# Kernel tuning notes

Hardware: AMD Instinct MI355X
Metric: run time of the kernel (lower is better)

Reference implementation:

```python
import jax, jax.numpy as jnp
import numpy as np

METRIC = (1.0, 1.0, 1.0, 1.0, -1.0)  # Cl(4,1) signature
N_HEADS = 8
EPS = 1e-6


def _cayley():
    # Cayley table C[a, b, k]: e_a * e_b = sum_k C[a,b,k] e_k, blades indexed by bitmask over 5 generators.
    C = np.zeros((32, 32, 32), dtype=np.float32)
    for a in range(32):
        for b in range(32):
            s = 0
            t = a >> 1
            while t:
                s += bin(t & b).count('1')
                t >>= 1
            sign = -1.0 if (s & 1) else 1.0
            for i in range(5):
                if (a & b) >> i & 1:
                    sign *= METRIC[i]
            C[a, b, a ^ b] = sign
    return C

_C_NP = _cayley()
GP_MAP = jnp.asarray(_C_NP)  # (32,32,32)
SIG = jnp.asarray(_C_NP[np.arange(32), np.arange(32), 0])  # blade square signs, (32,)


def normalize_cl41(x):
    # normalize each multivector (last-dim 32 blades) to unit RMS
    return x / jnp.sqrt(jnp.mean(x * x, axis=-1, keepdims=True) + EPS)


def versor_linear(x, W):
    # x: (B,S,I,32), W: (O,I,32); out_k = sum_{i,j,l} W[o,i,j] C[j,l,k] x[b,s,i,l]
    O, I, _ = W.shape
    W_op = jnp.einsum('oij,jlk->oilk', W, GP_MAP)  # (O,I,32,32)
    W_mat = W_op.transpose(1, 2, 0, 3).reshape(I * 32, O * 32)
    B, S = x.shape[0], x.shape[1]
    out = (x.reshape(B, S, I * 32) @ W_mat).reshape(B, S, O, 32)
    return normalize_cl41(out)


def versor_attention(x, Wq, Wk, Wv, Wo, lam):
    B, S, D, _ = x.shape
    H = N_HEADS
    hd = D // H

    def split_heads(t):  # (B,S,D,32) -> (B,H,S,hd,32)
        return t.reshape(B, S, H, hd, 32).transpose(0, 2, 1, 3, 4)

    q = split_heads(versor_linear(x, Wq))
    k = split_heads(versor_linear(x, Wk))
    v = split_heads(versor_linear(x, Wv))

    q_flat = (q * SIG).reshape(B, H, S, hd * 32)  # signature-weighted
    k_flat = k.reshape(B, H, S, hd * 32)

    scalar = jnp.einsum('bhsd,bhtd->bhst', q_flat, k_flat)
    scale = 1.0 / jnp.sqrt(jnp.asarray(hd, x.dtype))
    score = scalar * scale

    # torque term: sqrt(relu(|q|^2 |k|^2 - (q.k)^2) + eps) / sqrt(hd)
    q_norm_sq = jnp.sum(q_flat * q_flat, axis=-1)[..., :, None]  # (B,H,S,1)
    k_norm_sq = jnp.sum(k_flat * k_flat, axis=-1)[..., None, :]  # (B,H,1,S)
    torque = jnp.sqrt(jax.nn.relu(q_norm_sq * k_norm_sq - scalar * scalar) + EPS) * scale
    score = score + lam * torque

    probs = jax.nn.softmax(score, axis=-1)
    out = jnp.einsum('bhst,bhtdl->bhsdl', probs, v)  # (B,H,S,hd,32)
    out = out.transpose(0, 2, 1, 3, 4).reshape(B, S, D, 32)
    return versor_linear(out, Wo)


def setup_inputs() -> dict:
    key = jax.random.key(0)
    ks = jax.random.split(key, 5)
    B, S, D = 2, 1024, 128
    std = (2.0 / (D * 32)) ** 0.5  # Versor init
    x = jax.random.normal(ks[0], (B, S, D, 32), jnp.float32)
    Wq = jax.random.normal(ks[1], (D, D, 32), jnp.float32) * std
    Wk = jax.random.normal(ks[2], (D, D, 32), jnp.float32) * std
    Wv = jax.random.normal(ks[3], (D, D, 32), jnp.float32) * std
    Wo = jax.random.normal(ks[4], (D, D, 32), jnp.float32) * std
    attn_lambda = jnp.float32(0.1)
    return {'x': x, 'Wq': Wq, 'Wk': Wk, 'Wv': Wv, 'Wo': Wo, 'attn_lambda': attn_lambda}


def reference(x, Wq, Wk, Wv, Wo, attn_lambda):
    return versor_attention(x, Wq, Wk, Wv, Wo, attn_lambda)
```

## Files before the change

### kernel.cpp

```cpp
#include <hip/hip_runtime.h>
#include <stdint.h>

typedef __attribute__((ext_vector_type(4))) float    f32x4;
typedef __attribute__((ext_vector_type(8))) short    s16x8;
typedef __attribute__((ext_vector_type(4))) short    s16x4;
typedef __attribute__((ext_vector_type(8))) _Float16 f16x8;

#define DEV __device__ __forceinline__

DEV float blade_sign(int a, int b){
    int s = 0, t = a >> 1;
    while (t){ s += __popc(t & b); t >>= 1; }
    float sg = (s & 1) ? -1.0f : 1.0f;
    return ((a & b) & 16) ? -sg : sg;
}
DEV short f2h(float v){
    _Float16 h = (_Float16)v;
    return __builtin_bit_cast(short, h);
}
DEV float h2f(short b){
    return (float)__builtin_bit_cast(_Float16, b);
}

__global__ __launch_bounds__(256) void cast_f32_f16(const float* __restrict__ in,
                                                    short* __restrict__ out){
    const size_t idx = (size_t)blockIdx.x * 256 + threadIdx.x;
    const float4* p = reinterpret_cast<const float4*>(in) + idx * 2;
    float4 a = p[0], b = p[1];
    s16x8 o;
    o[0]=f2h(a.x); o[1]=f2h(a.y); o[2]=f2h(a.z); o[3]=f2h(a.w);
    o[4]=f2h(b.x); o[5]=f2h(b.y); o[6]=f2h(b.z); o[7]=f2h(b.w);
    *reinterpret_cast<s16x8*>(out + idx * 8) = o;
}

__global__ __launch_bounds__(256) void build_wmat(const float* __restrict__ W,
                                                  short* __restrict__ WmT){
    const int idx = blockIdx.x * 256 + threadIdx.x;
    const int n  = idx >> 9;
    const int kg = idx & 511;
    const int o = n >> 5, kb = n & 31;
    const int i = kg >> 2, l0 = (kg & 3) * 8;
    const float* wrow = W + (size_t)(o * 128 + i) * 32;
    s16x8 v;
    #pragma unroll
    for (int e = 0; e < 8; ++e){
        const int l = l0 + e, j = kb ^ l;
        v[e] = f2h(wrow[j] * blade_sign(j, l));
    }
    *reinterpret_cast<s16x8*>(WmT + (size_t)n * 4096 + kg * 8) = v;
}

__global__ __launch_bounds__(256) void row_norms(const short* __restrict__ Q,
                                                 const short* __restrict__ Kq,
                                                 float* __restrict__ Nq,
                                                 float* __restrict__ Nk){
    const int row  = blockIdx.x * 4 + (threadIdx.x >> 6);
    const int lane = threadIdx.x & 63;
    const int b = row >> 13, h = (row >> 10) & 7, s = row & 1023;
    const size_t off = ((size_t)(b * 1024 + s)) * 4096 + h * 512 + lane * 8;
    s16x8 a = *reinterpret_cast<const s16x8*>(Q + off);
    s16x8 c = *reinterpret_cast<const s16x8*>(Kq + off);
    float sq = 0.f, sk = 0.f;
    #pragma unroll
    for (int e = 0; e < 8; ++e){
        float fa = h2f(a[e]); sq = fmaf(fa, fa, sq);
        float fc = h2f(c[e]); sk = fmaf(fc, fc, sk);
    }
    #pragma unroll
    for (int m = 1; m < 64; m <<= 1){
        sq += __shfl_xor(sq, m);
        sk += __shfl_xor(sk, m);
    }
    if (lane == 0){ Nq[row] = sq; Nk[row] = sk; }
}

__global__ __launch_bounds__(256) void softmax_rows(float* __restrict__ Sc){
    const int row  = blockIdx.x * 4 + (threadIdx.x >> 6);
    const int lane = threadIdx.x & 63;
    float* p = Sc + (size_t)row * 1024;
    float v[16];
    float mx = -3.0e38f;
    #pragma unroll
    for (int j = 0; j < 16; ++j){ v[j] = p[lane + j * 64]; mx = fmaxf(mx, v[j]); }
    #pragma unroll
    for (int m = 1; m < 64; m <<= 1) mx = fmaxf(mx, __shfl_xor(mx, m));
    float sum = 0.f;
    #pragma unroll
    for (int j = 0; j < 16; ++j){ v[j] = __expf(v[j] - mx); sum += v[j]; }
    #pragma unroll
    for (int m = 1; m < 64; m <<= 1) sum += __shfl_xor(sum, m);
    const float inv = 1.0f / sum;
    short* pb = reinterpret_cast<short*>(p);
    #pragma unroll
    for (int j = 0; j < 16; ++j) pb[lane + j * 64] = f2h(v[j] * inv);
}

#define GLOAD_LDS(gp, lp) \
    __builtin_amdgcn_global_load_lds( \
        (const __attribute__((address_space(1))) void*)(const void*)(gp), \
        (__attribute__((address_space(3))) void*)(void*)(lp), 16, 0, 0)

template<int EPI>
__global__ __launch_bounds__(256) void versor_gemm(
    const short* __restrict__ Abase, int lda,
    const short* __restrict__ Bbase, int ldb,
    int K, void* __restrict__ OutP,
    const float* __restrict__ NqP, const float* __restrict__ NkP,
    const float* __restrict__ LamP)
{
    __shared__ short As[128 * 32];
    __shared__ short Bs[128 * 32];

    const int tid  = threadIdx.x;
    const int lane = tid & 63;
    const int wid  = tid >> 6;
    const int wr   = wid >> 1;
    const int wc   = wid & 1;
    const int bn = blockIdx.x, bm = blockIdx.y, z = blockIdx.z;

    const short* A = Abase;
    const short* B = Bbase;
    if constexpr (EPI == 4){
        const int b = z >> 3, h = z & 7;
        const size_t off = (size_t)b * 1024 * 4096 + (size_t)h * 512;
        A += off; B += off;
    }
    if constexpr (EPI == 5){
        A += (size_t)z * 1024 * 2048;
        B += (size_t)z * 512 * 1024;
    }

    const int row0 = bm * 128;
    const int col0 = bn * 128;

    const int slot0 = (wid * 2 + 0) * 64 + lane;
    const int slot1 = (wid * 2 + 1) * 64 + lane;
    const int ar0 = slot0 >> 2, ac0 = (slot0 & 3) * 8;
    const int ar1 = slot1 >> 2, ac1 = (slot1 & 3) * 8;
    const short* gA0 = A + (size_t)(row0 + ar0) * lda + ac0;
    const short* gA1 = A + (size_t)(row0 + ar1) * lda + ac1;
    const short* gB0 = B + (size_t)(col0 + ar0) * ldb + ac0;
    const short* gB1 = B + (size_t)(col0 + ar1) * ldb + ac1;
    short* lA0 = As + (wid * 2 + 0) * 512;
    short* lA1 = As + (wid * 2 + 1) * 512;
    short* lB0 = Bs + (wid * 2 + 0) * 512;
    short* lB1 = Bs + (wid * 2 + 1) * 512;

    f32x4 acc[4][4];
    #pragma unroll
    for (int i = 0; i < 4; ++i)
        #pragma unroll
        for (int j = 0; j < 4; ++j)
            acc[i][j] = (f32x4){0.f, 0.f, 0.f, 0.f};

    const int fragoff = (lane & 15) * 32 + (lane >> 4) * 8;

    for (int kt = 0; kt < K; kt += 32){
        __syncthreads();
        GLOAD_LDS(gA0 + kt, lA0);
        GLOAD_LDS(gA1 + kt, lA1);
        GLOAD_LDS(gB0 + kt, lB0);
        GLOAD_LDS(gB1 + kt, lB1);
        __syncthreads();

        f16x8 af[4], bfv[4];
        #pragma unroll
        for (int i = 0; i < 4; ++i){
            af[i]  = *reinterpret_cast<const f16x8*>(As + (wr * 64 + i * 16) * 32 + fragoff);
            bfv[i] = *reinterpret_cast<const f16x8*>(Bs + (wc * 64 + i * 16) * 32 + fragoff);
        }
        #pragma unroll
        for (int mi = 0; mi < 4; ++mi)
            #pragma unroll
            for (int ni = 0; ni < 4; ++ni)
                acc[mi][ni] = __builtin_amdgcn_mfma_f32_16x16x32_f16(
                    af[mi], bfv[ni], acc[mi][ni], 0, 0, 0);
    }

    const int rb = row0 + wr * 64 + (lane >> 4) * 4;
    const int cb = col0 + wc * 64 + (lane & 15);

    if constexpr (EPI <= 3){
        #pragma unroll
        for (int mi = 0; mi < 4; ++mi){
            #pragma unroll
            for (int g = 0; g < 2; ++g){
                f32x4 a0 = acc[mi][2 * g], a1 = acc[mi][2 * g + 1];
                f32x4 ss = a0 * a0 + a1 * a1;
                #pragma unroll
                for (int m = 1; m < 16; m <<= 1){
                    ss.x += __shfl_xor(ss.x, m);
                    ss.y += __shfl_xor(ss.y, m);
                    ss.z += __shfl_xor(ss.z, m);
                    ss.w += __shfl_xor(ss.w, m);
                }
                f32x4 inv;
                inv.x = 1.0f / sqrtf(ss.x * 0.03125f + 1e-6f);
                inv.y = 1.0f / sqrtf(ss.y * 0.03125f + 1e-6f);
                inv.z = 1.0f / sqrtf(ss.z * 0.03125f + 1e-6f);
                inv.w = 1.0f / sqrtf(ss.w * 0.03125f + 1e-6f);
                acc[mi][2 * g]     = a0 * inv;
                acc[mi][2 * g + 1] = a1 * inv;
            }
        }
    }
    if constexpr (EPI == 1){
        const float sg0 = blade_sign(lane & 15, lane & 15);
        const float sg1 = blade_sign(16 | (lane & 15), 16 | (lane & 15));
        #pragma unroll
        for (int mi = 0; mi < 4; ++mi)
            #pragma unroll
            for (int ni = 0; ni < 4; ++ni)
                acc[mi][ni] *= (ni & 1) ? sg1 : sg0;
    }

    if constexpr (EPI == 0 || EPI == 1){
        short* Ob = (short*)OutP;
        #pragma unroll
        for (int mi = 0; mi < 4; ++mi)
            #pragma unroll
            for (int ni = 0; ni < 4; ++ni)
                #pragma unroll
                for (int j = 0; j < 4; ++j)
                    Ob[(size_t)(rb + mi * 16 + j) * 4096 + (cb + ni * 16)] = f2h(acc[mi][ni][j]);
    }
    if constexpr (EPI == 2){
        short* Ob = (short*)OutP;
        #pragma unroll
        for (int mi = 0; mi < 4; ++mi){
            const int r = rb + mi * 16;
            const int b = r >> 10, t = r & 1023;
            #pragma unroll
            for (int ni = 0; ni < 4; ++ni){
                const int c = cb + ni * 16;
                const int h = c >> 9, f = c & 511;
                s16x4 pv;
                #pragma unroll
                for (int j = 0; j < 4; ++j) pv[j] = f2h(acc[mi][ni][j]);
                *reinterpret_cast<s16x4*>(Ob + ((size_t)((b * 8 + h) * 512 + f)) * 1024 + t) = pv;
            }
        }
    }
    if constexpr (EPI == 3){
        float* Of = (float*)OutP;
        #pragma unroll
        for (int mi = 0; mi < 4; ++mi)
            #pragma unroll
            for (int ni = 0; ni < 4; ++ni)
                #pragma unroll
                for (int j = 0; j < 4; ++j)
                    Of[(size_t)(rb + mi * 16 + j) * 4096 + (cb + ni * 16)] = acc[mi][ni][j];
    }
    if constexpr (EPI == 4){
        float* Of = (float*)OutP + (size_t)z * 1024 * 1024;
        const float lam = *LamP;
        const float* nq = NqP + z * 1024;
        const float* nk = NkP + z * 1024;
        #pragma unroll
        for (int mi = 0; mi < 4; ++mi)
            #pragma unroll
            for (int j = 0; j < 4; ++j){
                const int r = rb + mi * 16 + j;
                const float qn = nq[r];
                #pragma unroll
                for (int ni = 0; ni < 4; ++ni){
                    const int c = cb + ni * 16;
                    const float sc = acc[mi][ni][j];
                    const float tq = sqrtf(fmaxf(qn * nk[c] - sc * sc, 0.0f) + 1e-6f);
                    Of[(size_t)r * 1024 + c] = 0.25f * (sc + lam * tq);
                }
            }
    }
    if constexpr (EPI == 5){
        short* Ob = (short*)OutP;
        const int b = z >> 3, h = z & 7;
        #pragma unroll
        for (int mi = 0; mi < 4; ++mi)
            #pragma unroll
            for (int ni = 0; ni < 4; ++ni)
                #pragma unroll
                for (int j = 0; j < 4; ++j)
                    Ob[(size_t)(b * 1024 + rb + mi * 16 + j) * 4096 + h * 512 + (cb + ni * 16)]
                        = f2h(acc[mi][ni][j]);
    }
}

extern "C" void kernel_launch(void* const* d_in, const int* in_sizes, int n_in,
                              void* d_out, int out_size, void* d_ws, size_t ws_size,
                              hipStream_t stream)
{
    (void)in_sizes; (void)n_in; (void)out_size; (void)ws_size;
    const float* x   = (const float*)d_in[0];
    const float* Wq  = (const float*)d_in[1];
    const float* Wk  = (const float*)d_in[2];
    const float* Wv  = (const float*)d_in[3];
    const float* Wo  = (const float*)d_in[4];
    const float* lam = (const float*)d_in[5];
    float* out = (float*)d_out;
    char*  ws  = (char*)d_ws;

    short* Xf  = (short*)(ws);
    short* WmT = (short*)(ws + (16u << 20));
    short* Qf  = (short*)(ws + (48u << 20));
    short* Kf  = (short*)(ws + (64u << 20));
    short* Vt  = (short*)(ws + (80u << 20));
    float* Nq  = (float*)(ws + (96u << 20));
    float* Nk  = (float*)(ws + (96u << 20) + (1u << 20));
    float* Sc  = (float*)(ws + (98u << 20));

    dim3 blk(256);
    cast_f32_f16<<<4096, blk, 0, stream>>>(x, Xf);

    dim3 gproj(32, 16, 1);
    build_wmat<<<8192, blk, 0, stream>>>(Wq, WmT);
    versor_gemm<1><<<gproj, blk, 0, stream>>>(Xf, 4096, WmT, 4096, 4096, Qf, nullptr, nullptr, nullptr);
    build_wmat<<<8192, blk, 0, stream>>>(Wk, WmT);
    versor_gemm<0><<<gproj, blk, 0, stream>>>(Xf, 4096, WmT, 4096, 4096, Kf, nullptr, nullptr, nullptr);
    build_wmat<<<8192, blk, 0, stream>>>(Wv, WmT);
    versor_gemm<2><<<gproj, blk, 0, stream>>>(Xf, 4096, WmT, 4096, 4096, Vt, nullptr, nullptr, nullptr);

    row_norms<<<4096, blk, 0, stream>>>(Qf, Kf, Nq, Nk);

    dim3 gsc(8, 8, 16);
    versor_gemm<4><<<gsc, blk, 0, stream>>>(Qf, 4096, Kf, 4096, 512, Sc, Nq, Nk, lam);
    softmax_rows<<<4096, blk, 0, stream>>>(Sc);

    dim3 gpv(4, 8, 16);
    versor_gemm<5><<<gpv, blk, 0, stream>>>((const short*)Sc, 2048, Vt, 1024, 1024, Xf, nullptr, nullptr, nullptr);

    build_wmat<<<8192, blk, 0, stream>>>(Wo, WmT);
    versor_gemm<3><<<gproj, blk, 0, stream>>>(Xf, 4096, WmT, 4096, 4096, out, nullptr, nullptr, nullptr);
}
```

Baseline: 650.4 us.

## Batch Q/K/V weight builds and projections into single fused launches

Builds the three Q, K and V operator matrices in one launch and runs the three projection GEMMs as one grid with z selecting the weight and epilogue. This gives each launch 3x more blocks (1536 instead of 512) to fill the GPU and removes launch gaps between dependent kernels. It also lets the X tiles be shared in L2 across the three projections. Workspace is relaid out so all three weight matrices coexist, with the score buffer aliased over them after use. Common GEMM code is factored into macros.

```diff
diff --git a/kernel.cpp b/kernel.cpp
--- a/kernel.cpp
+++ b/kernel.cpp
@@ -33,9 +33,8 @@
     *reinterpret_cast<s16x8*>(out + idx * 8) = o;
 }
 
-__global__ __launch_bounds__(256) void build_wmat(const float* __restrict__ W,
-                                                  short* __restrict__ WmT){
-    const int idx = blockIdx.x * 256 + threadIdx.x;
+DEV void build_wmat_body(const float* __restrict__ W, short* __restrict__ WmT,
+                         int idx){
     const int n  = idx >> 9;
     const int kg = idx & 511;
     const int o = n >> 5, kb = n & 31;
@@ -48,6 +47,21 @@
         v[e] = f2h(wrow[j] * blade_sign(j, l));
     }
     *reinterpret_cast<s16x8*>(WmT + (size_t)n * 4096 + kg * 8) = v;
+}
+
+__global__ __launch_bounds__(256) void build_wmat(const float* __restrict__ W,
+                                                  short* __restrict__ WmT){
+    build_wmat_body(W, WmT, blockIdx.x * 256 + threadIdx.x);
+}
+
+__global__ __launch_bounds__(256) void build_wmat3(const float* __restrict__ Wq,
+                                                   const float* __restrict__ Wk,
+                                                   const float* __restrict__ Wv,
+                                                   short* __restrict__ WmT3){
+    const int w = blockIdx.y;
+    const float* W = (w == 0) ? Wq : ((w == 1) ? Wk : Wv);
+    build_wmat_body(W, WmT3 + (size_t)w * 4096 * 4096,
+                    blockIdx.x * 256 + threadIdx.x);
 }
 
 __global__ __launch_bounds__(256) void row_norms(const short* __restrict__ Q,
@@ -100,6 +114,138 @@
         (const __attribute__((address_space(1))) void*)(const void*)(gp), \
         (__attribute__((address_space(3))) void*)(void*)(lp), 16, 0, 0)
 
+#define GEMM_PROLOGUE(Aptr, ldA, Bptr, ldB)                                     \
+    __shared__ short As[128 * 32];                                              \
+    __shared__ short Bs[128 * 32];                                              \
+    const int tid  = threadIdx.x;                                               \
+    const int lane = tid & 63;                                                  \
+    const int wid  = tid >> 6;                                                  \
+    const int wr   = wid >> 1;                                                  \
+    const int wc   = wid & 1;                                                   \
+    const int row0 = blockIdx.y * 128;                                          \
+    const int col0 = blockIdx.x * 128;                                          \
+    const int slot0 = (wid * 2 + 0) * 64 + lane;                                \
+    const int slot1 = (wid * 2 + 1) * 64 + lane;                                \
+    const int ar0 = slot0 >> 2, ac0 = (slot0 & 3) * 8;                          \
+    const int ar1 = slot1 >> 2, ac1 = (slot1 & 3) * 8;                          \
+    const short* gA0 = (Aptr) + (size_t)(row0 + ar0) * (ldA) + ac0;             \
+    const short* gA1 = (Aptr) + (size_t)(row0 + ar1) * (ldA) + ac1;             \
+    const short* gB0 = (Bptr) + (size_t)(col0 + ar0) * (ldB) + ac0;             \
+    const short* gB1 = (Bptr) + (size_t)(col0 + ar1) * (ldB) + ac1;             \
+    short* lA0 = As + (wid * 2 + 0) * 512;                                      \
+    short* lA1 = As + (wid * 2 + 1) * 512;                                      \
+    short* lB0 = Bs + (wid * 2 + 0) * 512;                                      \
+    short* lB1 = Bs + (wid * 2 + 1) * 512;                                      \
+    f32x4 acc[4][4];                                                            \
+    _Pragma("unroll")                                                           \
+    for (int i = 0; i < 4; ++i)                                                 \
+        _Pragma("unroll")                                                       \
+        for (int j = 0; j < 4; ++j)                                             \
+            acc[i][j] = (f32x4){0.f, 0.f, 0.f, 0.f};                            \
+    const int fragoff = (lane & 15) * 32 + (lane >> 4) * 8;
+
+#define GEMM_KLOOP(Kdim)                                                        \
+    for (int kt = 0; kt < (Kdim); kt += 32){                                    \
+        __syncthreads();                                                        \
+        GLOAD_LDS(gA0 + kt, lA0);                                               \
+        GLOAD_LDS(gA1 + kt, lA1);                                               \
+        GLOAD_LDS(gB0 + kt, lB0);                                               \
+        GLOAD_LDS(gB1 + kt, lB1);                                               \
+        __syncthreads();                                                        \
+        f16x8 af[4], bfv[4];                                                    \
+        _Pragma("unroll")                                                       \
+        for (int i = 0; i < 4; ++i){                                            \
+            af[i]  = *reinterpret_cast<const f16x8*>(As + (wr*64 + i*16)*32 + fragoff); \
+            bfv[i] = *reinterpret_cast<const f16x8*>(Bs + (wc*64 + i*16)*32 + fragoff); \
+        }                                                                       \
+        _Pragma("unroll")                                                       \
+        for (int mi = 0; mi < 4; ++mi)                                          \
+            _Pragma("unroll")                                                   \
+            for (int ni = 0; ni < 4; ++ni)                                      \
+                acc[mi][ni] = __builtin_amdgcn_mfma_f32_16x16x32_f16(           \
+                    af[mi], bfv[ni], acc[mi][ni], 0, 0, 0);                     \
+    }
+
+#define GEMM_NORMALIZE()                                                        \
+    _Pragma("unroll")                                                           \
+    for (int mi = 0; mi < 4; ++mi){                                             \
+        _Pragma("unroll")                                                       \
+        for (int g = 0; g < 2; ++g){                                            \
+            f32x4 a0 = acc[mi][2*g], a1 = acc[mi][2*g+1];                       \
+            f32x4 ss = a0*a0 + a1*a1;                                           \
+            _Pragma("unroll")                                                   \
+            for (int m = 1; m < 16; m <<= 1){                                   \
+                ss.x += __shfl_xor(ss.x, m);                                    \
+                ss.y += __shfl_xor(ss.y, m);                                    \
+                ss.z += __shfl_xor(ss.z, m);                                    \
+                ss.w += __shfl_xor(ss.w, m);                                    \
+            }                                                                   \
+            f32x4 inv;                                                          \
+            inv.x = 1.0f / sqrtf(ss.x * 0.03125f + 1e-6f);                      \
+            inv.y = 1.0f / sqrtf(ss.y * 0.03125f + 1e-6f);                      \
+            inv.z = 1.0f / sqrtf(ss.z * 0.03125f + 1e-6f);                      \
+            inv.w = 1.0f / sqrtf(ss.w * 0.03125f + 1e-6f);                      \
+            acc[mi][2*g]   = a0 * inv;                                          \
+            acc[mi][2*g+1] = a1 * inv;                                          \
+        }                                                                       \
+    }
+
+__global__ __launch_bounds__(256) void versor_gemm_qkv(
+    const short* __restrict__ Xf,
+    const short* __restrict__ WmT3,
+    short* __restrict__ Qf,
+    short* __restrict__ Kf,
+    short* __restrict__ Vt)
+{
+    const int z = blockIdx.z;
+    const short* Bp = WmT3 + (size_t)z * 4096 * 4096;
+
+    GEMM_PROLOGUE(Xf, 4096, Bp, 4096)
+    GEMM_KLOOP(4096)
+
+    const int rb = row0 + wr * 64 + (lane >> 4) * 4;
+    const int cb = col0 + wc * 64 + (lane & 15);
+
+    GEMM_NORMALIZE()
+
+    if (z == 0){
+        const float sg0 = blade_sign(lane & 15, lane & 15);
+        const float sg1 = blade_sign(16 | (lane & 15), 16 | (lane & 15));
+        #pragma unroll
+        for (int mi = 0; mi < 4; ++mi)
+            #pragma unroll
+            for (int ni = 0; ni < 4; ++ni){
+                const f32x4 v = acc[mi][ni] * ((ni & 1) ? sg1 : sg0);
+                #pragma unroll
+                for (int j = 0; j < 4; ++j)
+                    Qf[(size_t)(rb + mi * 16 + j) * 4096 + (cb + ni * 16)] = f2h(v[j]);
+            }
+    } else if (z == 1){
+        #pragma unroll
+        for (int mi = 0; mi < 4; ++mi)
+            #pragma unroll
+            for (int ni = 0; ni < 4; ++ni)
+                #pragma unroll
+                for (int j = 0; j < 4; ++j)
+                    Kf[(size_t)(rb + mi * 16 + j) * 4096 + (cb + ni * 16)] = f2h(acc[mi][ni][j]);
+    } else {
+        #pragma unroll
+        for (int mi = 0; mi < 4; ++mi){
+            const int r = rb + mi * 16;
+            const int b = r >> 10, t = r & 1023;
+            #pragma unroll
+            for (int ni = 0; ni < 4; ++ni){
+                const int c = cb + ni * 16;
+                const int h = c >> 9, f = c & 511;
+                s16x4 pv;
+                #pragma unroll
+                for (int j = 0; j < 4; ++j) pv[j] = f2h(acc[mi][ni][j]);
+                *reinterpret_cast<s16x4*>(Vt + ((size_t)((b * 8 + h) * 512 + f)) * 1024 + t) = pv;
+            }
+        }
+    }
+}
+
 template<int EPI>
 __global__ __launch_bounds__(256) void versor_gemm(
     const short* __restrict__ Abase, int lda,
@@ -108,16 +254,7 @@
     const float* __restrict__ NqP, const float* __restrict__ NkP,
     const float* __restrict__ LamP)
 {
-    __shared__ short As[128 * 32];
-    __shared__ short Bs[128 * 32];
-
-    const int tid  = threadIdx.x;
-    const int lane = tid & 63;
-    const int wid  = tid >> 6;
-    const int wr   = wid >> 1;
-    const int wc   = wid & 1;
-    const int bn = blockIdx.x, bm = blockIdx.y, z = blockIdx.z;
-
+    const int z = blockIdx.z;
     const short* A = Abase;
     const short* B = Bbase;
     if constexpr (EPI == 4){
@@ -130,118 +267,14 @@
         B += (size_t)z * 512 * 1024;
     }
 
-    const int row0 = bm * 128;
-    const int col0 = bn * 128;
-
-    const int slot0 = (wid * 2 + 0) * 64 + lane;
-    const int slot1 = (wid * 2 + 1) * 64 + lane;
-    const int ar0 = slot0 >> 2, ac0 = (slot0 & 3) * 8;
-    const int ar1 = slot1 >> 2, ac1 = (slot1 & 3) * 8;
-    const short* gA0 = A + (size_t)(row0 + ar0) * lda + ac0;
-    const short* gA1 = A + (size_t)(row0 + ar1) * lda + ac1;
-    const short* gB0 = B + (size_t)(col0 + ar0) * ldb + ac0;
-    const short* gB1 = B + (size_t)(col0 + ar1) * ldb + ac1;
-    short* lA0 = As + (wid * 2 + 0) * 512;
-    short* lA1 = As + (wid * 2 + 1) * 512;
-    short* lB0 = Bs + (wid * 2 + 0) * 512;
-    short* lB1 = Bs + (wid * 2 + 1) * 512;
-
-    f32x4 acc[4][4];
-    #pragma unroll
-    for (int i = 0; i < 4; ++i)
-        #pragma unroll
-        for (int j = 0; j < 4; ++j)
-            acc[i][j] = (f32x4){0.f, 0.f, 0.f, 0.f};
-
-    const int fragoff = (lane & 15) * 32 + (lane >> 4) * 8;
-
-    for (int kt = 0; kt < K; kt += 32){
-        __syncthreads();
-        GLOAD_LDS(gA0 + kt, lA0);
-        GLOAD_LDS(gA1 + kt, lA1);
-        GLOAD_LDS(gB0 + kt, lB0);
-        GLOAD_LDS(gB1 + kt, lB1);
-        __syncthreads();
-
-        f16x8 af[4], bfv[4];
-        #pragma unroll
-        for (int i = 0; i < 4; ++i){
-            af[i]  = *reinterpret_cast<const f16x8*>(As + (wr * 64 + i * 16) * 32 + fragoff);
-            bfv[i] = *reinterpret_cast<const f16x8*>(Bs + (wc * 64 + i * 16) * 32 + fragoff);
-        }
-        #pragma unroll
-        for (int mi = 0; mi < 4; ++mi)
-            #pragma unroll
-            for (int ni = 0; ni < 4; ++ni)
-                acc[mi][ni] = __builtin_amdgcn_mfma_f32_16x16x32_f16(
-                    af[mi], bfv[ni], acc[mi][ni], 0, 0, 0);
-    }
+    GEMM_PROLOGUE(A, lda, B, ldb)
+    GEMM_KLOOP(K)
 
     const int rb = row0 + wr * 64 + (lane >> 4) * 4;
     const int cb = col0 + wc * 64 + (lane & 15);
 
-    if constexpr (EPI <= 3){
-        #pragma unroll
-        for (int mi = 0; mi < 4; ++mi){
-            #pragma unroll
-            for (int g = 0; g < 2; ++g){
-                f32x4 a0 = acc[mi][2 * g], a1 = acc[mi][2 * g + 1];
-                f32x4 ss = a0 * a0 + a1 * a1;
-                #pragma unroll
-                for (int m = 1; m < 16; m <<= 1){
-                    ss.x += __shfl_xor(ss.x, m);
-                    ss.y += __shfl_xor(ss.y, m);
-                    ss.z += __shfl_xor(ss.z, m);
-                    ss.w += __shfl_xor(ss.w, m);
-                }
-                f32x4 inv;
-                inv.x = 1.0f / sqrtf(ss.x * 0.03125f + 1e-6f);
-                inv.y = 1.0f / sqrtf(ss.y * 0.03125f + 1e-6f);
-                inv.z = 1.0f / sqrtf(ss.z * 0.03125f + 1e-6f);
-                inv.w = 1.0f / sqrtf(ss.w * 0.03125f + 1e-6f);
-                acc[mi][2 * g]     = a0 * inv;
-                acc[mi][2 * g + 1] = a1 * inv;
-            }
-        }
-    }
-    if constexpr (EPI == 1){
-        const float sg0 = blade_sign(lane & 15, lane & 15);
-        const float sg1 = blade_sign(16 | (lane & 15), 16 | (lane & 15));
-        #pragma unroll
-        for (int mi = 0; mi < 4; ++mi)
-            #pragma unroll
-            for (int ni = 0; ni < 4; ++ni)
-                acc[mi][ni] *= (ni & 1) ? sg1 : sg0;
-    }
-
-    if constexpr (EPI == 0 || EPI == 1){
-        short* Ob = (short*)OutP;
-        #pragma unroll
-        for (int mi = 0; mi < 4; ++mi)
-            #pragma unroll
-            for (int ni = 0; ni < 4; ++ni)
-                #pragma unroll
-                for (int j = 0; j < 4; ++j)
-                    Ob[(size_t)(rb + mi * 16 + j) * 4096 + (cb + ni * 16)] = f2h(acc[mi][ni][j]);
-    }
-    if constexpr (EPI == 2){
-        short* Ob = (short*)OutP;
-        #pragma unroll
-        for (int mi = 0; mi < 4; ++mi){
-            const int r = rb + mi * 16;
-            const int b = r >> 10, t = r & 1023;
-            #pragma unroll
-            for (int ni = 0; ni < 4; ++ni){
-                const int c = cb + ni * 16;
-                const int h = c >> 9, f = c & 511;
-                s16x4 pv;
-                #pragma unroll
-                for (int j = 0; j < 4; ++j) pv[j] = f2h(acc[mi][ni][j]);
-                *reinterpret_cast<s16x4*>(Ob + ((size_t)((b * 8 + h) * 512 + f)) * 1024 + t) = pv;
-            }
-        }
-    }
     if constexpr (EPI == 3){
+        GEMM_NORMALIZE()
         float* Of = (float*)OutP;
         #pragma unroll
         for (int mi = 0; mi < 4; ++mi)
@@ -299,35 +332,39 @@
     float* out = (float*)d_out;
     char*  ws  = (char*)d_ws;
 
-    short* Xf  = (short*)(ws);
-    short* WmT = (short*)(ws + (16u << 20));
-    short* Qf  = (short*)(ws + (48u << 20));
-    short* Kf  = (short*)(ws + (64u << 20));
-    short* Vt  = (short*)(ws + (80u << 20));
-    float* Nq  = (float*)(ws + (96u << 20));
-    float* Nk  = (float*)(ws + (96u << 20) + (1u << 20));
-    float* Sc  = (float*)(ws + (98u << 20));
+    short* Xf   = (short*)(ws);
+    short* WmT3 = (short*)(ws + (16u  << 20));
+    short* Qf   = (short*)(ws + (112u << 20));
+    short* Kf   = (short*)(ws + (128u << 20));
+    short* Vt   = (short*)(ws + (144u << 20));
+    float* Nq   = (float*)(ws + (160u << 20));
+    float* Nk   = (float*)(ws + (160u << 20) + (64u << 10));
+    float* Sc   = (float*)(ws + (16u  << 20));
+    short* WmTo = (short*)(ws + (80u  << 20));
+    short* Attn = Xf;
 
     dim3 blk(256);
     cast_f32_f16<<<4096, blk, 0, stream>>>(x, Xf);
 
-    dim3 gproj(32, 16, 1);
-    build_wmat<<<8192, blk, 0, stream>>>(Wq, WmT);
-    versor_gemm<1><<<gproj, blk, 0, stream>>>(Xf, 4096, WmT, 4096, 4096, Qf, nullptr, nullptr, nullptr);
-    build_wmat<<<8192, blk, 0, stream>>>(Wk, WmT);
-    versor_gemm<0><<<gproj, blk, 0, stream>>>(Xf, 4096, WmT, 4096, 4096, Kf, nullptr, nullptr, nullptr);
-    build_wmat<<<8192, blk, 0, stream>>>(Wv, WmT);
-    versor_gemm<2><<<gproj, blk, 0, stream>>>(Xf, 4096, WmT, 4096, 4096, Vt, nullptr, nullptr, nullptr);
+    dim3 gw3(8192, 3);
+    build_wmat3<<<gw3, blk, 0, stream>>>(Wq, Wk, Wv, WmT3);
+
+    dim3 gqkv(32, 16, 3);
+    versor_gemm_qkv<<<gqkv, blk, 0, stream>>>(Xf, WmT3, Qf, Kf, Vt);
 
     row_norms<<<4096, blk, 0, stream>>>(Qf, Kf, Nq, Nk);
+
+    build_wmat<<<8192, blk, 0, stream>>>(Wo, WmTo);
 
     dim3 gsc(8, 8, 16);
     versor_gemm<4><<<gsc, blk, 0, stream>>>(Qf, 4096, Kf, 4096, 512, Sc, Nq, Nk, lam);
     softmax_rows<<<4096, blk, 0, stream>>>(Sc);
 
     dim3 gpv(4, 8, 16);
-    versor_gemm<5><<<gpv, blk, 0, stream>>>((const short*)Sc, 2048, Vt, 1024, 1024, Xf, nullptr, nullptr, nullptr);
-
-    build_wmat<<<8192, blk, 0, stream>>>(Wo, WmT);
-    versor_gemm<3><<<gproj, blk, 0, stream>>>(Xf, 4096, WmT, 4096, 4096, out, nullptr, nullptr, nullptr);
-}
+    versor_gemm<5><<<gpv, blk, 0, stream>>>((const short*)Sc, 2048, Vt, 1024, 1024, Attn,
+                                            nullptr, nullptr, nullptr);
+
+    dim3 gproj(32, 16, 1);
+    versor_gemm<3><<<gproj, blk, 0, stream>>>(Attn, 4096, WmTo, 4096, 4096, out,
+                                              nullptr, nullptr, nullptr);
+}
```

Result: faster. 612.0 us (-5.9%).

## Fuse QKV projections into one 256x256 multi-stage pipelined GEMM

Applied to the files above, without the earlier changes.

Builds all three projection weight matrices in one launch and runs Q, K and V as a single GEMM over a concatenated weight matrix. The output projection and score GEMMs move to a new 512-thread kernel with 256x256 tiles, a 4-buffer global-to-LDS prefetch pipeline, swizzled LDS layout and MFMA priority hints. The PV GEMM keeps the old kernel. This cuts launches and raises data reuse per tile, at the cost of 128KB of LDS per block and fewer blocks for the smaller GEMMs.

```diff
diff --git a/kernel.cpp b/kernel.cpp
--- a/kernel.cpp
+++ b/kernel.cpp
@@ -33,9 +33,8 @@
     *reinterpret_cast<s16x8*>(out + idx * 8) = o;
 }
 
-__global__ __launch_bounds__(256) void build_wmat(const float* __restrict__ W,
-                                                  short* __restrict__ WmT){
-    const int idx = blockIdx.x * 256 + threadIdx.x;
+DEV void build_wmat_body(const float* __restrict__ W, short* __restrict__ WmT,
+                         int idx){
     const int n  = idx >> 9;
     const int kg = idx & 511;
     const int o = n >> 5, kb = n & 31;
@@ -48,6 +47,21 @@
         v[e] = f2h(wrow[j] * blade_sign(j, l));
     }
     *reinterpret_cast<s16x8*>(WmT + (size_t)n * 4096 + kg * 8) = v;
+}
+
+__global__ __launch_bounds__(256) void build_wmat(const float* __restrict__ W,
+                                                  short* __restrict__ WmT){
+    build_wmat_body(W, WmT, blockIdx.x * 256 + threadIdx.x);
+}
+
+__global__ __launch_bounds__(256) void build_wmat3(const float* __restrict__ Wq,
+                                                   const float* __restrict__ Wk,
+                                                   const float* __restrict__ Wv,
+                                                   short* __restrict__ WmT3){
+    const int w = blockIdx.y;
+    const float* W = (w == 0) ? Wq : ((w == 1) ? Wk : Wv);
+    build_wmat_body(W, WmT3 + (size_t)w * 4096 * 4096,
+                    blockIdx.x * 256 + threadIdx.x);
 }
 
 __global__ __launch_bounds__(256) void row_norms(const short* __restrict__ Q,
@@ -101,22 +115,22 @@
         (__attribute__((address_space(3))) void*)(void*)(lp), 16, 0, 0)
 
 template<int EPI>
-__global__ __launch_bounds__(256) void versor_gemm(
+__global__ __launch_bounds__(512, 2) void versor_gemm8(
     const short* __restrict__ Abase, int lda,
     const short* __restrict__ Bbase, int ldb,
     int K, void* __restrict__ OutP,
     const float* __restrict__ NqP, const float* __restrict__ NkP,
-    const float* __restrict__ LamP)
+    const float* __restrict__ LamP,
+    short* __restrict__ OQ, short* __restrict__ OK, short* __restrict__ OV)
 {
-    __shared__ short As[128 * 32];
-    __shared__ short Bs[128 * 32];
+    extern __shared__ short lds[];
 
     const int tid  = threadIdx.x;
     const int lane = tid & 63;
     const int wid  = tid >> 6;
-    const int wr   = wid >> 1;
-    const int wc   = wid & 1;
-    const int bn = blockIdx.x, bm = blockIdx.y, z = blockIdx.z;
+    const int wm   = wid >> 2;
+    const int wn   = wid & 3;
+    const int z    = blockIdx.z;
 
     const short* A = Abase;
     const short* B = Bbase;
@@ -125,64 +139,91 @@
         const size_t off = (size_t)b * 1024 * 4096 + (size_t)h * 512;
         A += off; B += off;
     }
-    if constexpr (EPI == 5){
-        A += (size_t)z * 1024 * 2048;
-        B += (size_t)z * 512 * 1024;
-    }
-
-    const int row0 = bm * 128;
-    const int col0 = bn * 128;
-
-    const int slot0 = (wid * 2 + 0) * 64 + lane;
-    const int slot1 = (wid * 2 + 1) * 64 + lane;
-    const int ar0 = slot0 >> 2, ac0 = (slot0 & 3) * 8;
-    const int ar1 = slot1 >> 2, ac1 = (slot1 & 3) * 8;
-    const short* gA0 = A + (size_t)(row0 + ar0) * lda + ac0;
-    const short* gA1 = A + (size_t)(row0 + ar1) * lda + ac1;
-    const short* gB0 = B + (size_t)(col0 + ar0) * ldb + ac0;
-    const short* gB1 = B + (size_t)(col0 + ar1) * ldb + ac1;
-    short* lA0 = As + (wid * 2 + 0) * 512;
-    short* lA1 = As + (wid * 2 + 1) * 512;
-    short* lB0 = Bs + (wid * 2 + 0) * 512;
-    short* lB1 = Bs + (wid * 2 + 1) * 512;
-
-    f32x4 acc[4][4];
-    #pragma unroll
-    for (int i = 0; i < 4; ++i)
+    const int row0 = blockIdx.y * 256;
+    const int col0 = blockIdx.x * 256;
+
+    const int jsw = ((lane & 3) ^ ((lane >> 3) & 3)) * 8;
+    const short* gA0 = A + (size_t)(row0 + wid * 32 + (lane >> 2)) * lda + jsw;
+    const short* gA1 = gA0 + (size_t)16 * lda;
+    const short* gB0 = B + (size_t)(col0 + wid * 32 + (lane >> 2)) * ldb + jsw;
+    const short* gB1 = gB0 + (size_t)16 * ldb;
+    const int dA0 = wid * 1024, dA1 = dA0 + 512;
+    const int dB0 = 8192 + wid * 1024, dB1 = dB0 + 512;
+
+    const int swz = ((lane >> 4) ^ (((lane & 15) >> 1) & 3)) * 8;
+    const int ard = (wm * 128 + (lane & 15)) * 32 + swz;
+    const int brd = 8192 + (wn * 64 + (lane & 15)) * 32 + swz;
+
+    f32x4 acc[8][4];
+    #pragma unroll
+    for (int i = 0; i < 8; ++i)
         #pragma unroll
         for (int j = 0; j < 4; ++j)
             acc[i][j] = (f32x4){0.f, 0.f, 0.f, 0.f};
 
-    const int fragoff = (lane & 15) * 32 + (lane >> 4) * 8;
-
-    for (int kt = 0; kt < K; kt += 32){
-        __syncthreads();
-        GLOAD_LDS(gA0 + kt, lA0);
-        GLOAD_LDS(gA1 + kt, lA1);
-        GLOAD_LDS(gB0 + kt, lB0);
-        GLOAD_LDS(gB1 + kt, lB1);
-        __syncthreads();
-
-        f16x8 af[4], bfv[4];
+    const int NT = K >> 5;
+
+    #pragma unroll
+    for (int pt = 0; pt < 3; ++pt){
+        const int bb = pt * 16384;
+        GLOAD_LDS(gA0 + pt * 32, lds + bb + dA0);
+        GLOAD_LDS(gA1 + pt * 32, lds + bb + dA1);
+        GLOAD_LDS(gB0 + pt * 32, lds + bb + dB0);
+        GLOAD_LDS(gB1 + pt * 32, lds + bb + dB1);
+    }
+
+    for (int t = 0; t < NT; ++t){
+        const int bb = (t & 3) * 16384;
+        asm volatile("s_waitcnt vmcnt(8)" ::: "memory");
+        __builtin_amdgcn_s_barrier();
+        asm volatile("" ::: "memory");
+        __builtin_amdgcn_sched_barrier(0);
+
+        if (t + 3 < NT){
+            const int nb = ((t + 3) & 3) * 16384;
+            GLOAD_LDS(gA0 + (t + 3) * 32, lds + nb + dA0);
+            GLOAD_LDS(gA1 + (t + 3) * 32, lds + nb + dA1);
+        }
+        f16x8 av[4], bv[4];
         #pragma unroll
         for (int i = 0; i < 4; ++i){
-            af[i]  = *reinterpret_cast<const f16x8*>(As + (wr * 64 + i * 16) * 32 + fragoff);
-            bfv[i] = *reinterpret_cast<const f16x8*>(Bs + (wc * 64 + i * 16) * 32 + fragoff);
-        }
+            av[i] = *reinterpret_cast<const f16x8*>(lds + bb + ard + i * 512);
+            bv[i] = *reinterpret_cast<const f16x8*>(lds + bb + brd + i * 512);
+        }
+        __builtin_amdgcn_s_setprio(1);
         #pragma unroll
         for (int mi = 0; mi < 4; ++mi)
             #pragma unroll
             for (int ni = 0; ni < 4; ++ni)
                 acc[mi][ni] = __builtin_amdgcn_mfma_f32_16x16x32_f16(
-                    af[mi], bfv[ni], acc[mi][ni], 0, 0, 0);
-    }
-
-    const int rb = row0 + wr * 64 + (lane >> 4) * 4;
-    const int cb = col0 + wc * 64 + (lane & 15);
-
-    if constexpr (EPI <= 3){
-        #pragma unroll
-        for (int mi = 0; mi < 4; ++mi){
+                    av[mi], bv[ni], acc[mi][ni], 0, 0, 0);
+        __builtin_amdgcn_s_setprio(0);
+
+        if (t + 3 < NT){
+            const int nb = ((t + 3) & 3) * 16384;
+            GLOAD_LDS(gB0 + (t + 3) * 32, lds + nb + dB0);
+            GLOAD_LDS(gB1 + (t + 3) * 32, lds + nb + dB1);
+        }
+        f16x8 aw[4];
+        #pragma unroll
+        for (int i = 0; i < 4; ++i)
+            aw[i] = *reinterpret_cast<const f16x8*>(lds + bb + ard + (4 + i) * 512);
+        __builtin_amdgcn_s_setprio(1);
+        #pragma unroll
+        for (int mi = 0; mi < 4; ++mi)
+            #pragma unroll
+            for (int ni = 0; ni < 4; ++ni)
+                acc[4 + mi][ni] = __builtin_amdgcn_mfma_f32_16x16x32_f16(
+                    aw[mi], bv[ni], acc[4 + mi][ni], 0, 0, 0);
+        __builtin_amdgcn_s_setprio(0);
+    }
+
+    const int rb = row0 + wm * 128 + (lane >> 4) * 4;
+    const int cb = col0 + wn * 64 + (lane & 15);
+
+    if constexpr (EPI == 0 || EPI == 3){
+        #pragma unroll
+        for (int mi = 0; mi < 8; ++mi){
             #pragma unroll
             for (int g = 0; g < 2; ++g){
                 f32x4 a0 = acc[mi][2 * g], a1 = acc[mi][2 * g + 1];
@@ -204,47 +245,51 @@
             }
         }
     }
-    if constexpr (EPI == 1){
-        const float sg0 = blade_sign(lane & 15, lane & 15);
-        const float sg1 = blade_sign(16 | (lane & 15), 16 | (lane & 15));
-        #pragma unroll
-        for (int mi = 0; mi < 4; ++mi)
-            #pragma unroll
-            for (int ni = 0; ni < 4; ++ni)
-                acc[mi][ni] *= (ni & 1) ? sg1 : sg0;
-    }
-
-    if constexpr (EPI == 0 || EPI == 1){
-        short* Ob = (short*)OutP;
-        #pragma unroll
-        for (int mi = 0; mi < 4; ++mi)
-            #pragma unroll
-            for (int ni = 0; ni < 4; ++ni)
-                #pragma unroll
-                for (int j = 0; j < 4; ++j)
-                    Ob[(size_t)(rb + mi * 16 + j) * 4096 + (cb + ni * 16)] = f2h(acc[mi][ni][j]);
-    }
-    if constexpr (EPI == 2){
-        short* Ob = (short*)OutP;
-        #pragma unroll
-        for (int mi = 0; mi < 4; ++mi){
-            const int r = rb + mi * 16;
-            const int b = r >> 10, t = r & 1023;
-            #pragma unroll
-            for (int ni = 0; ni < 4; ++ni){
-                const int c = cb + ni * 16;
-                const int h = c >> 9, f = c & 511;
-                s16x4 pv;
-                #pragma unroll
-                for (int j = 0; j < 4; ++j) pv[j] = f2h(acc[mi][ni][j]);
-                *reinterpret_cast<s16x4*>(Ob + ((size_t)((b * 8 + h) * 512 + f)) * 1024 + t) = pv;
+
+    if constexpr (EPI == 0){
+        const int zsel = col0 >> 12;
+        const int cbm  = (col0 & 4095) + wn * 64 + (lane & 15);
+        if (zsel == 0){
+            const float sg0 = blade_sign(lane & 15, lane & 15);
+            const float sg1 = blade_sign(16 | (lane & 15), 16 | (lane & 15));
+            #pragma unroll
+            for (int mi = 0; mi < 8; ++mi)
+                #pragma unroll
+                for (int ni = 0; ni < 4; ++ni){
+                    const f32x4 v = acc[mi][ni] * ((ni & 1) ? sg1 : sg0);
+                    #pragma unroll
+                    for (int j = 0; j < 4; ++j)
+                        OQ[(size_t)(rb + mi * 16 + j) * 4096 + (cbm + ni * 16)] = f2h(v[j]);
+                }
+        } else if (zsel == 1){
+            #pragma unroll
+            for (int mi = 0; mi < 8; ++mi)
+                #pragma unroll
+                for (int ni = 0; ni < 4; ++ni)
+                    #pragma unroll
+                    for (int j = 0; j < 4; ++j)
+                        OK[(size_t)(rb + mi * 16 + j) * 4096 + (cbm + ni * 16)] = f2h(acc[mi][ni][j]);
+        } else {
+            #pragma unroll
+            for (int mi = 0; mi < 8; ++mi){
+                const int r = rb + mi * 16;
+                const int b = r >> 10, tt = r & 1023;
+                #pragma unroll
+                for (int ni = 0; ni < 4; ++ni){
+                    const int c = cbm + ni * 16;
+                    const int h = c >> 9, f = c & 511;
+                    s16x4 pv;
+                    #pragma unroll
+                    for (int j = 0; j < 4; ++j) pv[j] = f2h(acc[mi][ni][j]);
+                    *reinterpret_cast<s16x4*>(OV + ((size_t)((b * 8 + h) * 512 + f)) * 1024 + tt) = pv;
+                }
             }
         }
     }
     if constexpr (EPI == 3){
         float* Of = (float*)OutP;
         #pragma unroll
-        for (int mi = 0; mi < 4; ++mi)
+        for (int mi = 0; mi < 8; ++mi)
             #pragma unroll
             for (int ni = 0; ni < 4; ++ni)
                 #pragma unroll
@@ -257,7 +302,7 @@
         const float* nq = NqP + z * 1024;
         const float* nk = NkP + z * 1024;
         #pragma unroll
-        for (int mi = 0; mi < 4; ++mi)
+        for (int mi = 0; mi < 8; ++mi)
             #pragma unroll
             for (int j = 0; j < 4; ++j){
                 const int r = rb + mi * 16 + j;
@@ -271,18 +316,84 @@
                 }
             }
     }
-    if constexpr (EPI == 5){
-        short* Ob = (short*)OutP;
-        const int b = z >> 3, h = z & 7;
+}
+
+__global__ __launch_bounds__(256) void versor_gemm_pv(
+    const short* __restrict__ Abase, int lda,
+    const short* __restrict__ Bbase, int ldb,
+    int K, short* __restrict__ OutP)
+{
+    __shared__ short As[128 * 32];
+    __shared__ short Bs[128 * 32];
+
+    const int tid  = threadIdx.x;
+    const int lane = tid & 63;
+    const int wid  = tid >> 6;
+    const int wr   = wid >> 1;
+    const int wc   = wid & 1;
+    const int z    = blockIdx.z;
+
+    const short* A = Abase + (size_t)z * 1024 * 2048;
+    const short* B = Bbase + (size_t)z * 512 * 1024;
+
+    const int row0 = blockIdx.y * 128;
+    const int col0 = blockIdx.x * 128;
+
+    const int slot0 = (wid * 2 + 0) * 64 + lane;
+    const int slot1 = (wid * 2 + 1) * 64 + lane;
+    const int ar0 = slot0 >> 2, ac0 = (slot0 & 3) * 8;
+    const int ar1 = slot1 >> 2, ac1 = (slot1 & 3) * 8;
+    const short* gA0 = A + (size_t)(row0 + ar0) * lda + ac0;
+    const short* gA1 = A + (size_t)(row0 + ar1) * lda + ac1;
+    const short* gB0 = B + (size_t)(col0 + ar0) * ldb + ac0;
+    const short* gB1 = B + (size_t)(col0 + ar1) * ldb + ac1;
+    short* lA0 = As + (wid * 2 + 0) * 512;
+    short* lA1 = As + (wid * 2 + 1) * 512;
+    short* lB0 = Bs + (wid * 2 + 0) * 512;
+    short* lB1 = Bs + (wid * 2 + 1) * 512;
+
+    f32x4 acc[4][4];
+    #pragma unroll
+    for (int i = 0; i < 4; ++i)
+        #pragma unroll
+        for (int j = 0; j < 4; ++j)
+            acc[i][j] = (f32x4){0.f, 0.f, 0.f, 0.f};
+
+    const int fragoff = (lane & 15) * 32 + (lane >> 4) * 8;
+
+    for (int kt = 0; kt < K; kt += 32){
+        __syncthreads();
+        GLOAD_LDS(gA0 + kt, lA0);
+        GLOAD_LDS(gA1 + kt, lA1);
+        GLOAD_LDS(gB0 + kt, lB0);
+        GLOAD_LDS(gB1 + kt, lB1);
+        __syncthreads();
+
+        f16x8 af[4], bfv[4];
+        #pragma unroll
+        for (int i = 0; i < 4; ++i){
+            af[i]  = *reinterpret_cast<const f16x8*>(As + (wr * 64 + i * 16) * 32 + fragoff);
+            bfv[i] = *reinterpret_cast<const f16x8*>(Bs + (wc * 64 + i * 16) * 32 + fragoff);
+        }
         #pragma unroll
         for (int mi = 0; mi < 4; ++mi)
             #pragma unroll
             for (int ni = 0; ni < 4; ++ni)
-                #pragma unroll
-                for (int j = 0; j < 4; ++j)
-                    Ob[(size_t)(b * 1024 + rb + mi * 16 + j) * 4096 + h * 512 + (cb + ni * 16)]
-                        = f2h(acc[mi][ni][j]);
-    }
+                acc[mi][ni] = __builtin_amdgcn_mfma_f32_16x16x32_f16(
+                    af[mi], bfv[ni], acc[mi][ni], 0, 0, 0);
+    }
+
+    const int rb = row0 + wr * 64 + (lane >> 4) * 4;
+    const int cb = col0 + wc * 64 + (lane & 15);
+    const int b = z >> 3, h = z & 7;
+    #pragma unroll
+    for (int mi = 0; mi < 4; ++mi)
+        #pragma unroll
+        for (int ni = 0; ni < 4; ++ni)
+            #pragma unroll
+            for (int j = 0; j < 4; ++j)
+                OutP[(size_t)(b * 1024 + rb + mi * 16 + j) * 4096 + h * 512 + (cb + ni * 16)]
+                    = f2h(acc[mi][ni][j]);
 }
 
 extern "C" void kernel_launch(void* const* d_in, const int* in_sizes, int n_in,
@@ -299,35 +410,48 @@
     float* out = (float*)d_out;
     char*  ws  = (char*)d_ws;
 
-    short* Xf  = (short*)(ws);
-    short* WmT = (short*)(ws + (16u << 20));
-    short* Qf  = (short*)(ws + (48u << 20));
-    short* Kf  = (short*)(ws + (64u << 20));
-    short* Vt  = (short*)(ws + (80u << 20));
-    float* Nq  = (float*)(ws + (96u << 20));
-    float* Nk  = (float*)(ws + (96u << 20) + (1u << 20));
-    float* Sc  = (float*)(ws + (98u << 20));
-
-    dim3 blk(256);
+    short* Xf   = (short*)(ws);
+    short* WmT3 = (short*)(ws + (16u  << 20));
+    short* Qf   = (short*)(ws + (112u << 20));
+    short* Kf   = (short*)(ws + (128u << 20));
+    short* Vt   = (short*)(ws + (144u << 20));
+    float* Nq   = (float*)(ws + (160u << 20));
+    float* Nk   = (float*)(ws + (160u << 20) + (64u << 10));
+    float* Sc   = (float*)(ws + (16u  << 20));
+    short* WmTo = (short*)(ws + (80u  << 20));
+    short* Attn = Xf;
+
+    const int DYN_LDS = 131072;
+    hipFuncSetAttribute(reinterpret_cast<const void*>(versor_gemm8<0>),
+                        hipFuncAttributeMaxDynamicSharedMemorySize, DYN_LDS);
+    hipFuncSetAttribute(reinterpret_cast<const void*>(versor_gemm8<3>),
+                        hipFuncAttributeMaxDynamicSharedMemorySize, DYN_LDS);
+    hipFuncSetAttribute(reinterpret_cast<const void*>(versor_gemm8<4>),
+                        hipFuncAttributeMaxDynamicSharedMemorySize, DYN_LDS);
+
+    dim3 blk(256), blk8(512);
     cast_f32_f16<<<4096, blk, 0, stream>>>(x, Xf);
 
-    dim3 gproj(32, 16, 1);
-    build_wmat<<<8192, blk, 0, stream>>>(Wq, WmT);
-    versor_gemm<1><<<gproj, blk, 0, stream>>>(Xf, 4096, WmT, 4096, 4096, Qf, nullptr, nullptr, nullptr);
-    build_wmat<<<8192, blk, 0, stream>>>(Wk, WmT);
-    versor_gemm<0><<<gproj, blk, 0, stream>>>(Xf, 4096, WmT, 4096, 4096, Kf, nullptr, nullptr, nullptr);
-    build_wmat<<<8192, blk, 0, stream>>>(Wv, WmT);
-    versor_gemm<2><<<gproj, blk, 0, stream>>>(Xf, 4096, WmT, 4096, 4096, Vt, nullptr, nullptr, nullptr);
+    dim3 gw3(8192, 3);
+    build_wmat3<<<gw3, blk, 0, stream>>>(Wq, Wk, Wv, WmT3);
+
+    dim3 gqkv(48, 8, 1);
+    versor_gemm8<0><<<gqkv, blk8, DYN_LDS, stream>>>(
+        Xf, 4096, WmT3, 4096, 4096, nullptr, nullptr, nullptr, nullptr, Qf, Kf, Vt);
 
     row_norms<<<4096, blk, 0, stream>>>(Qf, Kf, Nq, Nk);
 
-    dim3 gsc(8, 8, 16);
-    versor_gemm<4><<<gsc, blk, 0, stream>>>(Qf, 4096, Kf, 4096, 512, Sc, Nq, Nk, lam);
+    build_wmat<<<8192, blk, 0, stream>>>(Wo, WmTo);
+
+    dim3 gsc(4, 4, 16);
+    versor_gemm8<4><<<gsc, blk8, DYN_LDS, stream>>>(
+        Qf, 4096, Kf, 4096, 512, Sc, Nq, Nk, lam, nullptr, nullptr, nullptr);
     softmax_rows<<<4096, blk, 0, stream>>>(Sc);
 
     dim3 gpv(4, 8, 16);
-    versor_gemm<5><<<gpv, blk, 0, stream>>>((const short*)Sc, 2048, Vt, 1024, 1024, Xf, nullptr, nullptr, nullptr);
-
-    build_wmat<<<8192, blk, 0, stream>>>(Wo, WmT);
-    versor_gemm<3><<<gproj, blk, 0, stream>>>(Xf, 4096, WmT, 4096, 4096, out, nullptr, nullptr, nullptr);
-}
+    versor_gemm_pv<<<gpv, blk, 0, stream>>>((const short*)Sc, 2048, Vt, 1024, 1024, Attn);
+
+    dim3 gfin(16, 8, 1);
+    versor_gemm8<3><<<gfin, blk8, DYN_LDS, stream>>>(
+        Attn, 4096, WmTo, 4096, 4096, out, nullptr, nullptr, nullptr, nullptr, nullptr, nullptr);
+}
```

New measurement: 571.9 us. 12.1% less time.
